# Performance work log

Hardware: AMD Instinct MI355X
Metric: run time of the kernel (lower is better)

## Reference

```python
import jax, jax.numpy as jnp
import numpy as np

N_NODES = 50000
N_EDGES = 600000
F_DIM = 128


def setup_inputs() -> dict:
    key = jax.random.key(0)
    k_x, k_e, k_w1, k_b1, k_w2, k_b2 = jax.random.split(key, 6)
    x = jax.random.normal(k_x, (N_NODES, F_DIM), dtype=jnp.float32)
    edge_index = jax.random.randint(k_e, (2, N_EDGES), 0, N_NODES, dtype=jnp.int64)
    # nn.Linear-style params (weight is [out, in])
    s1 = 1.0 / np.sqrt(F_DIM)
    w1 = jax.random.uniform(k_w1, (128, F_DIM), jnp.float32, -s1, s1)
    b1 = jax.random.uniform(k_b1, (128,), jnp.float32, -s1, s1)
    s2 = 1.0 / np.sqrt(128)
    w2 = jax.random.uniform(k_w2, (F_DIM, 128), jnp.float32, -s2, s2)
    b2 = jax.random.uniform(k_b2, (F_DIM,), jnp.float32, -s2, s2)
    return {"x": x, "edge_index": edge_index, "w1": w1, "b1": b1, "w2": w2, "b2": b2}


def reference(x, edge_index, w1, b1, w2, b2):
    n = x.shape[0]
    # add_self_loops: append (i, i) for every node
    loops = jnp.arange(n, dtype=edge_index.dtype)
    src = jnp.concatenate([edge_index[0], loops])  # [E + N]
    dst = jnp.concatenate([edge_index[1], loops])  # [E + N]

    def conv(h):
        h = h @ w1.T + b1          # [N, 128]
        h = h @ w2.T + b2          # [N, F]
        msgs = h[src]              # gather source features [E+N, F]
        return jax.ops.segment_sum(msgs, dst, num_segments=n)  # scatter-add

    h = conv(conv(x))
    return jax.nn.log_softmax(h, axis=1)
```

## Files before the change

kernel.cpp:

```cpp
#include <hip/hip_runtime.h>
#include <hip/hip_bf16.h>

#define N_NODES 50000
#define N_EDGES 600000
#define F 128
#define BCAP 64

#define GEMM_BLOCKS 782
#define FILL_BLOCKS 2344

typedef unsigned short bf16_t;
typedef __attribute__((ext_vector_type(8))) short short8v;
typedef __attribute__((ext_vector_type(8))) unsigned short ushort8v;
typedef __attribute__((ext_vector_type(4))) float f32x4;

__device__ inline float bf2f(bf16_t u) {
    union { unsigned int i; float f; } c;
    c.i = ((unsigned int)u) << 16;
    return c.f;
}
__device__ inline bf16_t f2bf(float f) {
    union { float f; unsigned int i; } c;
    c.f = f;
    unsigned int lsb = (c.i >> 16) & 1;
    c.i += 0x7fffu + lsb;
    return (bf16_t)(c.i >> 16);
}

__global__ void k_fuse(const float* __restrict__ w1, const float* __restrict__ b1,
                       const float* __restrict__ w2, const float* __restrict__ b2,
                       float* __restrict__ Wc, float* __restrict__ bc,
                       int* __restrict__ cnt) {
    int p = blockIdx.x;
    int j = threadIdx.x;
    int gid = p * 128 + j;
    for (int i = gid; i < N_NODES; i += 128 * 128) cnt[i] = 0;

    float s = 0.f;
    for (int o = 0; o < F; ++o) s = fmaf(w2[p * F + o], w1[o * F + j], s);
    Wc[p * F + j] = s;
    if (j == 0) {
        float t = b2[p];
        for (int o = 0; o < F; ++o) t = fmaf(w2[p * F + o], b1[o], t);
        bc[p] = t;
    }
}

__global__ void k_fuse2(const float* __restrict__ Wc, const float* __restrict__ bc,
                        bf16_t* __restrict__ Mbf, float* __restrict__ v1) {
    int k = blockIdx.x;
    int p = threadIdx.x;
    float s = 0.f;
    for (int o = 0; o < F; ++o) s = fmaf(Wc[p * F + o], Wc[o * F + k], s);
    Mbf[p * F + k] = f2bf(s);
    if (k == 0) {
        float t = 0.f;
        for (int o = 0; o < F; ++o) t = fmaf(Wc[p * F + o], bc[o], t);
        v1[p] = t;
    }
}

__global__ __launch_bounds__(256, 4)
void k_main(const float* __restrict__ X, const bf16_t* __restrict__ Mbf,
            bf16_t* __restrict__ G,
            const int* __restrict__ src, const int* __restrict__ dst,
            int* __restrict__ cnt, unsigned short* __restrict__ bucket) {
    const int bid = blockIdx.x;
    const int tid = threadIdx.x;

    if (bid >= GEMM_BLOCKS) {
        int e = (bid - GEMM_BLOCKS) * 256 + tid;
        if (e < N_EDGES) {
            int d = dst[e];
            int slot = atomicAdd(&cnt[d], 1);
            if (slot < BCAP) bucket[d * BCAP + slot] = (unsigned short)src[e];
        }
        return;
    }

    __shared__ unsigned short Xs[64 * 128];
    const int row0 = bid * 64;

    for (int idx = tid; idx < 1024; idx += 256) {
        int r = idx >> 4, c = idx & 15;
        int grow = row0 + r;
        float4 va = {0.f, 0.f, 0.f, 0.f}, vb = {0.f, 0.f, 0.f, 0.f};
        if (grow < N_NODES) {
            const float4* xr = (const float4*)(X + (size_t)grow * F);
            va = xr[2 * c];
            vb = xr[2 * c + 1];
        }
        ushort8v u;
        u[0] = f2bf(va.x); u[1] = f2bf(va.y); u[2] = f2bf(va.z); u[3] = f2bf(va.w);
        u[4] = f2bf(vb.x); u[5] = f2bf(vb.y); u[6] = f2bf(vb.z); u[7] = f2bf(vb.w);
        *(ushort8v*)&Xs[r * 128 + (((c ^ (r & 7)) << 3))] = u;
    }
    __syncthreads();

    const int wid = tid >> 6;
    const int lane = tid & 63;
    const int wr = wid >> 1;
    const int wc = wid & 1;
    const int l15 = lane & 15;
    const int l4 = lane >> 4;
    const int sw = (l15 & 7);

    f32x4 acc[2][4] = {};

#pragma unroll
    for (int kc = 0; kc < 4; ++kc) {
        const int cS = ((kc * 4 + l4) ^ sw) << 3;
        short8v a0 = *(const short8v*)&Xs[(wr * 32 + 0 * 16 + l15) * 128 + cS];
        short8v a1 = *(const short8v*)&Xs[(wr * 32 + 1 * 16 + l15) * 128 + cS];
        const bf16_t* mb = Mbf + (size_t)(wc * 64 + l15) * F + kc * 32 + 8 * l4;
        short8v b0 = *(const short8v*)(mb + 0 * 16 * F);
        short8v b1 = *(const short8v*)(mb + 1 * 16 * F);
        short8v b2 = *(const short8v*)(mb + 2 * 16 * F);
        short8v b3 = *(const short8v*)(mb + 3 * 16 * F);
        acc[0][0] = __builtin_amdgcn_mfma_f32_16x16x32_bf16(a0, b0, acc[0][0], 0, 0, 0);
        acc[0][1] = __builtin_amdgcn_mfma_f32_16x16x32_bf16(a0, b1, acc[0][1], 0, 0, 0);
        acc[0][2] = __builtin_amdgcn_mfma_f32_16x16x32_bf16(a0, b2, acc[0][2], 0, 0, 0);
        acc[0][3] = __builtin_amdgcn_mfma_f32_16x16x32_bf16(a0, b3, acc[0][3], 0, 0, 0);
        acc[1][0] = __builtin_amdgcn_mfma_f32_16x16x32_bf16(a1, b0, acc[1][0], 0, 0, 0);
        acc[1][1] = __builtin_amdgcn_mfma_f32_16x16x32_bf16(a1, b1, acc[1][1], 0, 0, 0);
        acc[1][2] = __builtin_amdgcn_mfma_f32_16x16x32_bf16(a1, b2, acc[1][2], 0, 0, 0);
        acc[1][3] = __builtin_amdgcn_mfma_f32_16x16x32_bf16(a1, b3, acc[1][3], 0, 0, 0);
    }

#pragma unroll
    for (int mt = 0; mt < 2; ++mt) {
#pragma unroll
        for (int nt = 0; nt < 4; ++nt) {
#pragma unroll
            for (int r = 0; r < 4; ++r) {
                int grow = row0 + wr * 32 + mt * 16 + l4 * 4 + r;
                if (grow < N_NODES) {
                    int gcol = wc * 64 + nt * 16 + l15;
                    G[(size_t)grow * F + gcol] = f2bf(acc[mt][nt][r]);
                }
            }
        }
    }
}

__global__ __launch_bounds__(256)
void k_agg(const bf16_t* __restrict__ H, const int* __restrict__ cnt,
           const unsigned short* __restrict__ bucket, bf16_t* __restrict__ O,
           int n_rows) {
    int tid = threadIdx.x;
    int lane = tid & 31;
    int node = blockIdx.x * 8 + (tid >> 5);
    if (node >= n_rows) return;

    int deg = cnt[node];
    if (deg > BCAP) deg = BCAP;
    ushort4 u = ((const ushort4*)(H + (size_t)node * F))[lane];
    float a0 = bf2f(u.x), a1 = bf2f(u.y), a2 = bf2f(u.z), a3 = bf2f(u.w);

    const unsigned short* bk = bucket + node * BCAP;
    int i = 0;
    for (; i + 8 <= deg; i += 8) {
        ushort8v s8 = *(const ushort8v*)(bk + i);
        ushort4 u0 = ((const ushort4*)(H + (size_t)s8[0] * F))[lane];
        ushort4 u1 = ((const ushort4*)(H + (size_t)s8[1] * F))[lane];
        ushort4 u2 = ((const ushort4*)(H + (size_t)s8[2] * F))[lane];
        ushort4 u3 = ((const ushort4*)(H + (size_t)s8[3] * F))[lane];
        ushort4 u4 = ((const ushort4*)(H + (size_t)s8[4] * F))[lane];
        ushort4 u5 = ((const ushort4*)(H + (size_t)s8[5] * F))[lane];
        ushort4 u6 = ((const ushort4*)(H + (size_t)s8[6] * F))[lane];
        ushort4 u7 = ((const ushort4*)(H + (size_t)s8[7] * F))[lane];
        a0 += bf2f(u0.x) + bf2f(u1.x) + bf2f(u2.x) + bf2f(u3.x)
            + bf2f(u4.x) + bf2f(u5.x) + bf2f(u6.x) + bf2f(u7.x);
        a1 += bf2f(u0.y) + bf2f(u1.y) + bf2f(u2.y) + bf2f(u3.y)
            + bf2f(u4.y) + bf2f(u5.y) + bf2f(u6.y) + bf2f(u7.y);
        a2 += bf2f(u0.z) + bf2f(u1.z) + bf2f(u2.z) + bf2f(u3.z)
            + bf2f(u4.z) + bf2f(u5.z) + bf2f(u6.z) + bf2f(u7.z);
        a3 += bf2f(u0.w) + bf2f(u1.w) + bf2f(u2.w) + bf2f(u3.w)
            + bf2f(u4.w) + bf2f(u5.w) + bf2f(u6.w) + bf2f(u7.w);
    }
    for (; i + 4 <= deg; i += 4) {
        ushort4 s4 = *(const ushort4*)(bk + i);
        ushort4 u0 = ((const ushort4*)(H + (size_t)s4.x * F))[lane];
        ushort4 u1 = ((const ushort4*)(H + (size_t)s4.y * F))[lane];
        ushort4 u2 = ((const ushort4*)(H + (size_t)s4.z * F))[lane];
        ushort4 u3 = ((const ushort4*)(H + (size_t)s4.w * F))[lane];
        a0 += bf2f(u0.x) + bf2f(u1.x) + bf2f(u2.x) + bf2f(u3.x);
        a1 += bf2f(u0.y) + bf2f(u1.y) + bf2f(u2.y) + bf2f(u3.y);
        a2 += bf2f(u0.z) + bf2f(u1.z) + bf2f(u2.z) + bf2f(u3.z);
        a3 += bf2f(u0.w) + bf2f(u1.w) + bf2f(u2.w) + bf2f(u3.w);
    }
    for (; i < deg; ++i) {
        ushort4 uv = ((const ushort4*)(H + (size_t)bk[i] * F))[lane];
        a0 += bf2f(uv.x); a1 += bf2f(uv.y); a2 += bf2f(uv.z); a3 += bf2f(uv.w);
    }
    ushort4 o;
    o.x = f2bf(a0); o.y = f2bf(a1); o.z = f2bf(a2); o.w = f2bf(a3);
    ((ushort4*)(O + (size_t)node * F))[lane] = o;
}

__global__ __launch_bounds__(256)
void k_agg_ep(const bf16_t* __restrict__ H, const int* __restrict__ cnt,
              const unsigned short* __restrict__ bucket,
              const float* __restrict__ v1, const float* __restrict__ bc,
              float* __restrict__ O, int n_rows) {
    int tid = threadIdx.x;
    int lane = tid & 31;
    int node = blockIdx.x * 8 + (tid >> 5);
    if (node >= n_rows) return;

    int deg_t = cnt[node];
    int deg = deg_t < BCAP ? deg_t : BCAP;
    ushort4 u = ((const ushort4*)(H + (size_t)node * F))[lane];
    float a0 = bf2f(u.x), a1 = bf2f(u.y), a2 = bf2f(u.z), a3 = bf2f(u.w);

    const unsigned short* bk = bucket + node * BCAP;

    int sdi = (lane == 0) ? (deg_t + 1) : 0;
    for (int j = lane; j < deg; j += 32) sdi += cnt[bk[j]] + 1;

    int i = 0;
    for (; i + 8 <= deg; i += 8) {
        ushort8v s8 = *(const ushort8v*)(bk + i);
        ushort4 u0 = ((const ushort4*)(H + (size_t)s8[0] * F))[lane];
        ushort4 u1 = ((const ushort4*)(H + (size_t)s8[1] * F))[lane];
        ushort4 u2 = ((const ushort4*)(H + (size_t)s8[2] * F))[lane];
        ushort4 u3 = ((const ushort4*)(H + (size_t)s8[3] * F))[lane];
        ushort4 u4 = ((const ushort4*)(H + (size_t)s8[4] * F))[lane];
        ushort4 u5 = ((const ushort4*)(H + (size_t)s8[5] * F))[lane];
        ushort4 u6 = ((const ushort4*)(H + (size_t)s8[6] * F))[lane];
        ushort4 u7 = ((const ushort4*)(H + (size_t)s8[7] * F))[lane];
        a0 += bf2f(u0.x) + bf2f(u1.x) + bf2f(u2.x) + bf2f(u3.x)
            + bf2f(u4.x) + bf2f(u5.x) + bf2f(u6.x) + bf2f(u7.x);
        a1 += bf2f(u0.y) + bf2f(u1.y) + bf2f(u2.y) + bf2f(u3.y)
            + bf2f(u4.y) + bf2f(u5.y) + bf2f(u6.y) + bf2f(u7.y);
        a2 += bf2f(u0.z) + bf2f(u1.z) + bf2f(u2.z) + bf2f(u3.z)
            + bf2f(u4.z) + bf2f(u5.z) + bf2f(u6.z) + bf2f(u7.z);
        a3 += bf2f(u0.w) + bf2f(u1.w) + bf2f(u2.w) + bf2f(u3.w)
            + bf2f(u4.w) + bf2f(u5.w) + bf2f(u6.w) + bf2f(u7.w);
    }
    for (; i + 4 <= deg; i += 4) {
        ushort4 s4 = *(const ushort4*)(bk + i);
        ushort4 u0 = ((const ushort4*)(H + (size_t)s4.x * F))[lane];
        ushort4 u1 = ((const ushort4*)(H + (size_t)s4.y * F))[lane];
        ushort4 u2 = ((const ushort4*)(H + (size_t)s4.z * F))[lane];
        ushort4 u3 = ((const ushort4*)(H + (size_t)s4.w * F))[lane];
        a0 += bf2f(u0.x) + bf2f(u1.x) + bf2f(u2.x) + bf2f(u3.x);
        a1 += bf2f(u0.y) + bf2f(u1.y) + bf2f(u2.y) + bf2f(u3.y);
        a2 += bf2f(u0.z) + bf2f(u1.z) + bf2f(u2.z) + bf2f(u3.z);
        a3 += bf2f(u0.w) + bf2f(u1.w) + bf2f(u2.w) + bf2f(u3.w);
    }
    for (; i < deg; ++i) {
        ushort4 uv = ((const ushort4*)(H + (size_t)bk[i] * F))[lane];
        a0 += bf2f(uv.x); a1 += bf2f(uv.y); a2 += bf2f(uv.z); a3 += bf2f(uv.w);
    }

#pragma unroll
    for (int o = 16; o; o >>= 1) sdi += __shfl_xor(sdi, o);
    float sdn = (float)sdi;
    float dn = (float)(deg_t + 1);
    float4 v1v = ((const float4*)v1)[lane];
    float4 bcv = ((const float4*)bc)[lane];
    a0 += sdn * v1v.x + dn * bcv.x;
    a1 += sdn * v1v.y + dn * bcv.y;
    a2 += sdn * v1v.z + dn * bcv.z;
    a3 += sdn * v1v.w + dn * bcv.w;

    float m = fmaxf(fmaxf(a0, a1), fmaxf(a2, a3));
#pragma unroll
    for (int o = 16; o; o >>= 1) m = fmaxf(m, __shfl_xor(m, o));
    float s = expf(a0 - m) + expf(a1 - m) + expf(a2 - m) + expf(a3 - m);
#pragma unroll
    for (int o = 16; o; o >>= 1) s += __shfl_xor(s, o);
    float lse = m + logf(s);
    float4 o4;
    o4.x = a0 - lse; o4.y = a1 - lse; o4.z = a2 - lse; o4.w = a3 - lse;
    ((float4*)(O + (size_t)node * F))[lane] = o4;
}

extern "C" void kernel_launch(void* const* d_in, const int* in_sizes, int n_in,
                              void* d_out, int out_size, void* d_ws, size_t ws_size,
                              hipStream_t stream) {
    const float* x  = (const float*)d_in[0];
    const int* ei   = (const int*)d_in[1];
    const float* w1 = (const float*)d_in[2];
    const float* b1 = (const float*)d_in[3];
    const float* w2 = (const float*)d_in[4];
    const float* b2 = (const float*)d_in[5];
    float* out = (float*)d_out;

    const int* src = ei;
    const int* dst = ei + N_EDGES;

    float* ws        = (float*)d_ws;
    float* Wc        = ws;
    float* bc        = ws + 16384;
    float* v1        = ws + 16512;
    bf16_t* Mbf      = (bf16_t*)(ws + 16640);
    int*   cnt       = (int*)(ws + 24832);
    unsigned short* bucket = (unsigned short*)(ws + 74880);
    bf16_t* g        = (bf16_t*)(ws + 1674880);
    bf16_t* a1       = (bf16_t*)(ws + 4874880);

    const int node_grid = (N_NODES + 7) / 8;

    k_fuse<<<128, 128, 0, stream>>>(w1, b1, w2, b2, Wc, bc, cnt);
    k_fuse2<<<128, 128, 0, stream>>>(Wc, bc, Mbf, v1);

    k_main<<<GEMM_BLOCKS + FILL_BLOCKS, 256, 0, stream>>>(x, Mbf, g, src, dst,
                                                          cnt, bucket);
    k_agg<<<node_grid, 256, 0, stream>>>(g, cnt, bucket, a1, N_NODES);
    k_agg_ep<<<node_grid, 256, 0, stream>>>(a1, cnt, bucket, v1, bc, out, N_NODES);
}
```

Measured before the change: 121.1 us.

## Replace capped per-node buckets with exact CSR via count, scan, and fill

Replaces the fixed-capacity (64) per-node bucket adjacency with a true CSR. Edge counting now runs inside the weight-fusion kernel, and a single-block scan builds the row offsets. The fill step then writes into compact positions. The aggregation kernels switch from 32 lanes reading ushort4 to 16 lanes reading ushort8 per node, which halves the threads per node and gives contiguous index reads. In exchange it adds a kernel launch, a serial single-block scan, and a second atomic pass over the edges.

New measurement: 264.4 us. +118.4%, slower.

```diff
diff --git a/kernel.cpp b/kernel.cpp
--- a/kernel.cpp
+++ b/kernel.cpp
@@ -4,10 +4,9 @@
 #define N_NODES 50000
 #define N_EDGES 600000
 #define F 128
-#define BCAP 64
 
 #define GEMM_BLOCKS 782
-#define FILL_BLOCKS 2344
+#define EDGE_BLOCKS 2344
 
 typedef unsigned short bf16_t;
 typedef __attribute__((ext_vector_type(8))) short short8v;
@@ -46,17 +45,61 @@
     }
 }
 
-__global__ void k_fuse2(const float* __restrict__ Wc, const float* __restrict__ bc,
-                        bf16_t* __restrict__ Mbf, float* __restrict__ v1) {
-    int k = blockIdx.x;
-    int p = threadIdx.x;
-    float s = 0.f;
-    for (int o = 0; o < F; ++o) s = fmaf(Wc[p * F + o], Wc[o * F + k], s);
-    Mbf[p * F + k] = f2bf(s);
-    if (k == 0) {
-        float t = 0.f;
-        for (int o = 0; o < F; ++o) t = fmaf(Wc[p * F + o], bc[o], t);
-        v1[p] = t;
+__global__ __launch_bounds__(256)
+void k_fuse2h(const float* __restrict__ Wc, const float* __restrict__ bc,
+              bf16_t* __restrict__ Mbf, float* __restrict__ v1,
+              const int* __restrict__ dst, int* __restrict__ cnt) {
+    int bid = blockIdx.x;
+    int tid = threadIdx.x;
+    if (bid < 128) {
+        if (tid < 128) {
+            int k = bid, p = tid;
+            float s = 0.f;
+            for (int o = 0; o < F; ++o) s = fmaf(Wc[p * F + o], Wc[o * F + k], s);
+            Mbf[p * F + k] = f2bf(s);
+            if (k == 0) {
+                float t = 0.f;
+                for (int o = 0; o < F; ++o) t = fmaf(Wc[p * F + o], bc[o], t);
+                v1[p] = t;
+            }
+        }
+        return;
+    }
+    int e = (bid - 128) * 256 + tid;
+    if (e < N_EDGES) atomicAdd(&cnt[dst[e]], 1);
+}
+
+__global__ __launch_bounds__(1024)
+void k_scan(const int* __restrict__ cnt, int* __restrict__ rofs,
+            int* __restrict__ wofs) {
+    __shared__ int part[1024];
+    const int t = threadIdx.x;
+    const int CH = 49;
+    const int base = t * CH;
+
+    int s = 0;
+    for (int i = 0; i < CH; ++i) {
+        int idx = base + i;
+        if (idx < N_NODES) s += cnt[idx];
+    }
+    part[t] = s;
+    __syncthreads();
+    for (int off = 1; off < 1024; off <<= 1) {
+        int v = (t >= off) ? part[t - off] : 0;
+        __syncthreads();
+        part[t] += v;
+        __syncthreads();
+    }
+    int run = (t == 0) ? 0 : part[t - 1];
+    for (int i = 0; i < CH; ++i) {
+        int idx = base + i;
+        if (idx < N_NODES) {
+            rofs[idx] = run;
+            wofs[idx] = run;
+            run += cnt[idx];
+        } else if (idx == N_NODES) {
+            rofs[idx] = run;
+        }
     }
 }
 
@@ -64,7 +107,7 @@
 void k_main(const float* __restrict__ X, const bf16_t* __restrict__ Mbf,
             bf16_t* __restrict__ G,
             const int* __restrict__ src, const int* __restrict__ dst,
-            int* __restrict__ cnt, unsigned short* __restrict__ bucket) {
+            int* __restrict__ wofs, unsigned short* __restrict__ csr) {
     const int bid = blockIdx.x;
     const int tid = threadIdx.x;
 
@@ -72,8 +115,8 @@
         int e = (bid - GEMM_BLOCKS) * 256 + tid;
         if (e < N_EDGES) {
             int d = dst[e];
-            int slot = atomicAdd(&cnt[d], 1);
-            if (slot < BCAP) bucket[d * BCAP + slot] = (unsigned short)src[e];
+            int pos = atomicAdd(&wofs[d], 1);
+            csr[pos] = (unsigned short)src[e];
         }
         return;
     }
@@ -144,137 +187,122 @@
 }
 
 __global__ __launch_bounds__(256)
-void k_agg(const bf16_t* __restrict__ H, const int* __restrict__ cnt,
-           const unsigned short* __restrict__ bucket, bf16_t* __restrict__ O,
+void k_agg(const bf16_t* __restrict__ H, const int* __restrict__ rofs,
+           const unsigned short* __restrict__ csr, bf16_t* __restrict__ O,
            int n_rows) {
     int tid = threadIdx.x;
-    int lane = tid & 31;
-    int node = blockIdx.x * 8 + (tid >> 5);
+    int lane = tid & 15;
+    int node = blockIdx.x * 16 + (tid >> 4);
     if (node >= n_rows) return;
 
-    int deg = cnt[node];
-    if (deg > BCAP) deg = BCAP;
-    ushort4 u = ((const ushort4*)(H + (size_t)node * F))[lane];
-    float a0 = bf2f(u.x), a1 = bf2f(u.y), a2 = bf2f(u.z), a3 = bf2f(u.w);
-
-    const unsigned short* bk = bucket + node * BCAP;
+    int r0 = rofs[node];
+    int deg = rofs[node + 1] - r0;
+
+    ushort8v u = ((const ushort8v*)(H + (size_t)node * F))[lane];
+    float a0 = bf2f(u[0]), a1 = bf2f(u[1]), a2 = bf2f(u[2]), a3 = bf2f(u[3]);
+    float a4 = bf2f(u[4]), a5 = bf2f(u[5]), a6 = bf2f(u[6]), a7 = bf2f(u[7]);
+
+    const unsigned short* bk = csr + r0;
     int i = 0;
-    for (; i + 8 <= deg; i += 8) {
-        ushort8v s8 = *(const ushort8v*)(bk + i);
-        ushort4 u0 = ((const ushort4*)(H + (size_t)s8[0] * F))[lane];
-        ushort4 u1 = ((const ushort4*)(H + (size_t)s8[1] * F))[lane];
-        ushort4 u2 = ((const ushort4*)(H + (size_t)s8[2] * F))[lane];
-        ushort4 u3 = ((const ushort4*)(H + (size_t)s8[3] * F))[lane];
-        ushort4 u4 = ((const ushort4*)(H + (size_t)s8[4] * F))[lane];
-        ushort4 u5 = ((const ushort4*)(H + (size_t)s8[5] * F))[lane];
-        ushort4 u6 = ((const ushort4*)(H + (size_t)s8[6] * F))[lane];
-        ushort4 u7 = ((const ushort4*)(H + (size_t)s8[7] * F))[lane];
-        a0 += bf2f(u0.x) + bf2f(u1.x) + bf2f(u2.x) + bf2f(u3.x)
-            + bf2f(u4.x) + bf2f(u5.x) + bf2f(u6.x) + bf2f(u7.x);
-        a1 += bf2f(u0.y) + bf2f(u1.y) + bf2f(u2.y) + bf2f(u3.y)
-            + bf2f(u4.y) + bf2f(u5.y) + bf2f(u6.y) + bf2f(u7.y);
-        a2 += bf2f(u0.z) + bf2f(u1.z) + bf2f(u2.z) + bf2f(u3.z)
-            + bf2f(u4.z) + bf2f(u5.z) + bf2f(u6.z) + bf2f(u7.z);
-        a3 += bf2f(u0.w) + bf2f(u1.w) + bf2f(u2.w) + bf2f(u3.w)
-            + bf2f(u4.w) + bf2f(u5.w) + bf2f(u6.w) + bf2f(u7.w);
-    }
     for (; i + 4 <= deg; i += 4) {
-        ushort4 s4 = *(const ushort4*)(bk + i);
-        ushort4 u0 = ((const ushort4*)(H + (size_t)s4.x * F))[lane];
-        ushort4 u1 = ((const ushort4*)(H + (size_t)s4.y * F))[lane];
-        ushort4 u2 = ((const ushort4*)(H + (size_t)s4.z * F))[lane];
-        ushort4 u3 = ((const ushort4*)(H + (size_t)s4.w * F))[lane];
-        a0 += bf2f(u0.x) + bf2f(u1.x) + bf2f(u2.x) + bf2f(u3.x);
-        a1 += bf2f(u0.y) + bf2f(u1.y) + bf2f(u2.y) + bf2f(u3.y);
-        a2 += bf2f(u0.z) + bf2f(u1.z) + bf2f(u2.z) + bf2f(u3.z);
-        a3 += bf2f(u0.w) + bf2f(u1.w) + bf2f(u2.w) + bf2f(u3.w);
+        int s0 = bk[i + 0], s1 = bk[i + 1], s2 = bk[i + 2], s3 = bk[i + 3];
+        ushort8v u0 = ((const ushort8v*)(H + (size_t)s0 * F))[lane];
+        ushort8v u1 = ((const ushort8v*)(H + (size_t)s1 * F))[lane];
+        ushort8v u2 = ((const ushort8v*)(H + (size_t)s2 * F))[lane];
+        ushort8v u3 = ((const ushort8v*)(H + (size_t)s3 * F))[lane];
+        a0 += bf2f(u0[0]) + bf2f(u1[0]) + bf2f(u2[0]) + bf2f(u3[0]);
+        a1 += bf2f(u0[1]) + bf2f(u1[1]) + bf2f(u2[1]) + bf2f(u3[1]);
+        a2 += bf2f(u0[2]) + bf2f(u1[2]) + bf2f(u2[2]) + bf2f(u3[2]);
+        a3 += bf2f(u0[3]) + bf2f(u1[3]) + bf2f(u2[3]) + bf2f(u3[3]);
+        a4 += bf2f(u0[4]) + bf2f(u1[4]) + bf2f(u2[4]) + bf2f(u3[4]);
+        a5 += bf2f(u0[5]) + bf2f(u1[5]) + bf2f(u2[5]) + bf2f(u3[5]);
+        a6 += bf2f(u0[6]) + bf2f(u1[6]) + bf2f(u2[6]) + bf2f(u3[6]);
+        a7 += bf2f(u0[7]) + bf2f(u1[7]) + bf2f(u2[7]) + bf2f(u3[7]);
     }
     for (; i < deg; ++i) {
-        ushort4 uv = ((const ushort4*)(H + (size_t)bk[i] * F))[lane];
-        a0 += bf2f(uv.x); a1 += bf2f(uv.y); a2 += bf2f(uv.z); a3 += bf2f(uv.w);
-    }
-    ushort4 o;
-    o.x = f2bf(a0); o.y = f2bf(a1); o.z = f2bf(a2); o.w = f2bf(a3);
-    ((ushort4*)(O + (size_t)node * F))[lane] = o;
+        ushort8v uv = ((const ushort8v*)(H + (size_t)bk[i] * F))[lane];
+        a0 += bf2f(uv[0]); a1 += bf2f(uv[1]); a2 += bf2f(uv[2]); a3 += bf2f(uv[3]);
+        a4 += bf2f(uv[4]); a5 += bf2f(uv[5]); a6 += bf2f(uv[6]); a7 += bf2f(uv[7]);
+    }
+    ushort8v o;
+    o[0] = f2bf(a0); o[1] = f2bf(a1); o[2] = f2bf(a2); o[3] = f2bf(a3);
+    o[4] = f2bf(a4); o[5] = f2bf(a5); o[6] = f2bf(a6); o[7] = f2bf(a7);
+    ((ushort8v*)(O + (size_t)node * F))[lane] = o;
 }
 
 __global__ __launch_bounds__(256)
-void k_agg_ep(const bf16_t* __restrict__ H, const int* __restrict__ cnt,
-              const unsigned short* __restrict__ bucket,
+void k_agg_ep(const bf16_t* __restrict__ H, const int* __restrict__ rofs,
+              const unsigned short* __restrict__ csr, const int* __restrict__ cnt,
               const float* __restrict__ v1, const float* __restrict__ bc,
               float* __restrict__ O, int n_rows) {
     int tid = threadIdx.x;
-    int lane = tid & 31;
-    int node = blockIdx.x * 8 + (tid >> 5);
+    int lane = tid & 15;
+    int node = blockIdx.x * 16 + (tid >> 4);
     if (node >= n_rows) return;
 
-    int deg_t = cnt[node];
-    int deg = deg_t < BCAP ? deg_t : BCAP;
-    ushort4 u = ((const ushort4*)(H + (size_t)node * F))[lane];
-    float a0 = bf2f(u.x), a1 = bf2f(u.y), a2 = bf2f(u.z), a3 = bf2f(u.w);
-
-    const unsigned short* bk = bucket + node * BCAP;
-
-    int sdi = (lane == 0) ? (deg_t + 1) : 0;
-    for (int j = lane; j < deg; j += 32) sdi += cnt[bk[j]] + 1;
+    int r0 = rofs[node];
+    int deg = rofs[node + 1] - r0;
+
+    ushort8v u = ((const ushort8v*)(H + (size_t)node * F))[lane];
+    float a0 = bf2f(u[0]), a1 = bf2f(u[1]), a2 = bf2f(u[2]), a3 = bf2f(u[3]);
+    float a4 = bf2f(u[4]), a5 = bf2f(u[5]), a6 = bf2f(u[6]), a7 = bf2f(u[7]);
+
+    const unsigned short* bk = csr + r0;
+
+    int sdi = (lane == 0) ? (deg + 1) : 0;
+    for (int j = lane; j < deg; j += 16) sdi += cnt[bk[j]] + 1;
 
     int i = 0;
-    for (; i + 8 <= deg; i += 8) {
-        ushort8v s8 = *(const ushort8v*)(bk + i);
-        ushort4 u0 = ((const ushort4*)(H + (size_t)s8[0] * F))[lane];
-        ushort4 u1 = ((const ushort4*)(H + (size_t)s8[1] * F))[lane];
-        ushort4 u2 = ((const ushort4*)(H + (size_t)s8[2] * F))[lane];
-        ushort4 u3 = ((const ushort4*)(H + (size_t)s8[3] * F))[lane];
-        ushort4 u4 = ((const ushort4*)(H + (size_t)s8[4] * F))[lane];
-        ushort4 u5 = ((const ushort4*)(H + (size_t)s8[5] * F))[lane];
-        ushort4 u6 = ((const ushort4*)(H + (size_t)s8[6] * F))[lane];
-        ushort4 u7 = ((const ushort4*)(H + (size_t)s8[7] * F))[lane];
-        a0 += bf2f(u0.x) + bf2f(u1.x) + bf2f(u2.x) + bf2f(u3.x)
-            + bf2f(u4.x) + bf2f(u5.x) + bf2f(u6.x) + bf2f(u7.x);
-        a1 += bf2f(u0.y) + bf2f(u1.y) + bf2f(u2.y) + bf2f(u3.y)
-            + bf2f(u4.y) + bf2f(u5.y) + bf2f(u6.y) + bf2f(u7.y);
-        a2 += bf2f(u0.z) + bf2f(u1.z) + bf2f(u2.z) + bf2f(u3.z)
-            + bf2f(u4.z) + bf2f(u5.z) + bf2f(u6.z) + bf2f(u7.z);
-        a3 += bf2f(u0.w) + bf2f(u1.w) + bf2f(u2.w) + bf2f(u3.w)
-            + bf2f(u4.w) + bf2f(u5.w) + bf2f(u6.w) + bf2f(u7.w);
-    }
     for (; i + 4 <= deg; i += 4) {
-        ushort4 s4 = *(const ushort4*)(bk + i);
-        ushort4 u0 = ((const ushort4*)(H + (size_t)s4.x * F))[lane];
-        ushort4 u1 = ((const ushort4*)(H + (size_t)s4.y * F))[lane];
-        ushort4 u2 = ((const ushort4*)(H + (size_t)s4.z * F))[lane];
-        ushort4 u3 = ((const ushort4*)(H + (size_t)s4.w * F))[lane];
-        a0 += bf2f(u0.x) + bf2f(u1.x) + bf2f(u2.x) + bf2f(u3.x);
-        a1 += bf2f(u0.y) + bf2f(u1.y) + bf2f(u2.y) + bf2f(u3.y);
-        a2 += bf2f(u0.z) + bf2f(u1.z) + bf2f(u2.z) + bf2f(u3.z);
-        a3 += bf2f(u0.w) + bf2f(u1.w) + bf2f(u2.w) + bf2f(u3.w);
+        int s0 = bk[i + 0], s1 = bk[i + 1], s2 = bk[i + 2], s3 = bk[i + 3];
+        ushort8v u0 = ((const ushort8v*)(H + (size_t)s0 * F))[lane];
+        ushort8v u1 = ((const ushort8v*)(H + (size_t)s1 * F))[lane];
+        ushort8v u2 = ((const ushort8v*)(H + (size_t)s2 * F))[lane];
+        ushort8v u3 = ((const ushort8v*)(H + (size_t)s3 * F))[lane];
+        a0 += bf2f(u0[0]) + bf2f(u1[0]) + bf2f(u2[0]) + bf2f(u3[0]);
+        a1 += bf2f(u0[1]) + bf2f(u1[1]) + bf2f(u2[1]) + bf2f(u3[1]);
+        a2 += bf2f(u0[2]) + bf2f(u1[2]) + bf2f(u2[2]) + bf2f(u3[2]);
+        a3 += bf2f(u0[3]) + bf2f(u1[3]) + bf2f(u2[3]) + bf2f(u3[3]);
+        a4 += bf2f(u0[4]) + bf2f(u1[4]) + bf2f(u2[4]) + bf2f(u3[4]);
+        a5 += bf2f(u0[5]) + bf2f(u1[5]) + bf2f(u2[5]) + bf2f(u3[5]);
+        a6 += bf2f(u0[6]) + bf2f(u1[6]) + bf2f(u2[6]) + bf2f(u3[6]);
+        a7 += bf2f(u0[7]) + bf2f(u1[7]) + bf2f(u2[7]) + bf2f(u3[7]);
     }
     for (; i < deg; ++i) {
-        ushort4 uv = ((const ushort4*)(H + (size_t)bk[i] * F))[lane];
-        a0 += bf2f(uv.x); a1 += bf2f(uv.y); a2 += bf2f(uv.z); a3 += bf2f(uv.w);
-    }
-
-#pragma unroll
-    for (int o = 16; o; o >>= 1) sdi += __shfl_xor(sdi, o);
+        ushort8v uv = ((const ushort8v*)(H + (size_t)bk[i] * F))[lane];
+        a0 += bf2f(uv[0]); a1 += bf2f(uv[1]); a2 += bf2f(uv[2]); a3 += bf2f(uv[3]);
+        a4 += bf2f(uv[4]); a5 += bf2f(uv[5]); a6 += bf2f(uv[6]); a7 += bf2f(uv[7]);
+    }
+
+#pragma unroll
+    for (int o = 8; o; o >>= 1) sdi += __shfl_xor(sdi, o);
     float sdn = (float)sdi;
-    float dn = (float)(deg_t + 1);
-    float4 v1v = ((const float4*)v1)[lane];
-    float4 bcv = ((const float4*)bc)[lane];
-    a0 += sdn * v1v.x + dn * bcv.x;
-    a1 += sdn * v1v.y + dn * bcv.y;
-    a2 += sdn * v1v.z + dn * bcv.z;
-    a3 += sdn * v1v.w + dn * bcv.w;
-
-    float m = fmaxf(fmaxf(a0, a1), fmaxf(a2, a3));
-#pragma unroll
-    for (int o = 16; o; o >>= 1) m = fmaxf(m, __shfl_xor(m, o));
-    float s = expf(a0 - m) + expf(a1 - m) + expf(a2 - m) + expf(a3 - m);
-#pragma unroll
-    for (int o = 16; o; o >>= 1) s += __shfl_xor(s, o);
+    float dn = (float)(deg + 1);
+    float4 v1a = ((const float4*)v1)[2 * lane], v1b = ((const float4*)v1)[2 * lane + 1];
+    float4 bca = ((const float4*)bc)[2 * lane], bcb = ((const float4*)bc)[2 * lane + 1];
+    a0 += sdn * v1a.x + dn * bca.x;
+    a1 += sdn * v1a.y + dn * bca.y;
+    a2 += sdn * v1a.z + dn * bca.z;
+    a3 += sdn * v1a.w + dn * bca.w;
+    a4 += sdn * v1b.x + dn * bcb.x;
+    a5 += sdn * v1b.y + dn * bcb.y;
+    a6 += sdn * v1b.z + dn * bcb.z;
+    a7 += sdn * v1b.w + dn * bcb.w;
+
+    float m = fmaxf(fmaxf(fmaxf(a0, a1), fmaxf(a2, a3)),
+                    fmaxf(fmaxf(a4, a5), fmaxf(a6, a7)));
+#pragma unroll
+    for (int o = 8; o; o >>= 1) m = fmaxf(m, __shfl_xor(m, o));
+    float s = expf(a0 - m) + expf(a1 - m) + expf(a2 - m) + expf(a3 - m)
+            + expf(a4 - m) + expf(a5 - m) + expf(a6 - m) + expf(a7 - m);
+#pragma unroll
+    for (int o = 8; o; o >>= 1) s += __shfl_xor(s, o);
     float lse = m + logf(s);
-    float4 o4;
-    o4.x = a0 - lse; o4.y = a1 - lse; o4.z = a2 - lse; o4.w = a3 - lse;
-    ((float4*)(O + (size_t)node * F))[lane] = o4;
+    float4 oa, ob;
+    oa.x = a0 - lse; oa.y = a1 - lse; oa.z = a2 - lse; oa.w = a3 - lse;
+    ob.x = a4 - lse; ob.y = a5 - lse; ob.z = a6 - lse; ob.w = a7 - lse;
+    ((float4*)(O + (size_t)node * F))[2 * lane] = oa;
+    ((float4*)(O + (size_t)node * F))[2 * lane + 1] = ob;
 }
 
 extern "C" void kernel_launch(void* const* d_in, const int* in_sizes, int n_in,
@@ -291,23 +319,25 @@
     const int* src = ei;
     const int* dst = ei + N_EDGES;
 
-    float* ws        = (float*)d_ws;
-    float* Wc        = ws;
-    float* bc        = ws + 16384;
-    float* v1        = ws + 16512;
-    bf16_t* Mbf      = (bf16_t*)(ws + 16640);
-    int*   cnt       = (int*)(ws + 24832);
-    unsigned short* bucket = (unsigned short*)(ws + 74880);
-    bf16_t* g        = (bf16_t*)(ws + 1674880);
-    bf16_t* a1       = (bf16_t*)(ws + 4874880);
-
-    const int node_grid = (N_NODES + 7) / 8;
+    float* ws       = (float*)d_ws;
+    float* Wc       = ws;
+    float* bc       = ws + 16384;
+    float* v1       = ws + 16512;
+    bf16_t* Mbf     = (bf16_t*)(ws + 16640);
+    int*   cnt      = (int*)(ws + 24832);
+    int*   rofs     = (int*)(ws + 74880);
+    int*   wofs     = (int*)(ws + 124928);
+    unsigned short* csr = (unsigned short*)(ws + 174976);
+    bf16_t* g       = (bf16_t*)(ws + 474976);
+    bf16_t* a1      = (bf16_t*)(ws + 3674976);
+
+    const int node_grid = (N_NODES + 15) / 16;
 
     k_fuse<<<128, 128, 0, stream>>>(w1, b1, w2, b2, Wc, bc, cnt);
-    k_fuse2<<<128, 128, 0, stream>>>(Wc, bc, Mbf, v1);
-
-    k_main<<<GEMM_BLOCKS + FILL_BLOCKS, 256, 0, stream>>>(x, Mbf, g, src, dst,
-                                                          cnt, bucket);
-    k_agg<<<node_grid, 256, 0, stream>>>(g, cnt, bucket, a1, N_NODES);
-    k_agg_ep<<<node_grid, 256, 0, stream>>>(a1, cnt, bucket, v1, bc, out, N_NODES);
-}
+    k_fuse2h<<<128 + EDGE_BLOCKS, 256, 0, stream>>>(Wc, bc, Mbf, v1, dst, cnt);
+    k_scan<<<1, 1024, 0, stream>>>(cnt, rofs, wofs);
+    k_main<<<GEMM_BLOCKS + EDGE_BLOCKS, 256, 0, stream>>>(x, Mbf, g, src, dst,
+                                                          wofs, csr);
+    k_agg<<<node_grid, 256, 0, stream>>>(g, rofs, csr, a1, N_NODES);
+    k_agg_ep<<<node_grid, 256, 0, stream>>>(a1, rofs, csr, cnt, v1, bc, out, N_NODES);
+}
```
